# Kernel optimization log

Hardware: AMD Instinct MI355X
Metric: run time of the kernel (lower is better)

The kernel has to match this reference:

```python
import jax, jax.numpy as jnp
import numpy as np

NUM_TREE = 64
DEPTH = 7
INPUT_FEATURE = 1024
BATCH = 32768
LEAF = 2 ** (DEPTH - 1)  # 64


def setup_inputs() -> dict:
    key = jax.random.key(0)
    k1, k2 = jax.random.split(key, 2)
    x = jax.random.normal(k1, (BATCH, INPUT_FEATURE), dtype=jnp.float32)
    # each tree picks leaf_num-1 distinct feature columns (one-hot matmul == gather)
    rng = np.random.default_rng(0)
    idx = np.stack([rng.choice(INPUT_FEATURE, LEAF - 1, replace=False)
                    for _ in range(NUM_TREE)]).astype(np.int32)
    feature_idx = jnp.asarray(idx)  # [T, L-1]
    # pi.get_mean(): leaf means, np.random.rand -> uniform [0,1)
    pi = jax.random.uniform(k2, (NUM_TREE, LEAF), dtype=jnp.float32)
    return {"x": x, "feature_idx": feature_idx, "pi": pi}


def reference(x, feature_idx, pi):
    T, Lm1 = feature_idx.shape
    leaf = Lm1 + 1
    depth = int(np.log2(leaf)) + 1  # static
    B = x.shape[0]
    # torch.mm(x, one_hot_feature) == column gather; sigmoid routing decisions
    d = jax.nn.sigmoid(x[:, feature_idx])  # [B, T, L-1]
    # recursive cumulative-product leaf probabilities over tree layers (BFS order)
    mu = jnp.ones((B, T, 1), dtype=x.dtype)
    begin = 0
    for layer in range(depth - 1):
        n = 2 ** layer
        dl = d[:, :, begin:begin + n]  # [B, T, n]
        # child order per node: (left=sigmoid, right=1-sigmoid), interleaved
        mu = jnp.stack([mu * dl, mu * (1.0 - dl)], axis=-1).reshape(B, T, 2 * n)
        begin += n
    # mu: [B, T, L] leaf probabilities per tree
    prob = jnp.einsum('btl,tl->bt', mu, pi)        # [B, T]
    probs = jnp.transpose(mu, (0, 2, 1))           # [B, L, T] (matches torch layout)
    return prob, probs
```

## Files before the change

### kernel.cpp

```cpp
#include <hip/hip_runtime.h>

#define NTREE  64
#define NFEAT  1024
#define NLEAF  64
#define NBATCH 32768
#define WAVES  4
#define THREADS 256

__global__ __launch_bounds__(THREADS)
void forest_kernel(const float* __restrict__ x,
                   const int*   __restrict__ fidx,
                   const float* __restrict__ pi,
                   float* __restrict__ prob,
                   float* __restrict__ probs)
{
    __shared__ float srow[WAVES][NFEAT];
    __shared__ int   idxl[NTREE * 63];
    __shared__ float pil[NTREE * 65];

    const int tid  = threadIdx.x;
    const int wid  = tid >> 6;
    const int lane = tid & 63;

    for (int i = tid; i < NTREE * 63; i += THREADS) idxl[i] = fidx[i];
    for (int i = tid; i < NTREE * NLEAF; i += THREADS)
        pil[(i >> 6) * 65 + (i & 63)] = pi[i];
    __syncthreads();

    const int wavestride = gridDim.x * WAVES;
    for (int b = blockIdx.x * WAVES + wid; b < NBATCH; b += wavestride) {
        const float4* xr4 = reinterpret_cast<const float4*>(x + (size_t)b * NFEAT);
        float4* sr4 = reinterpret_cast<float4*>(&srow[wid][0]);
        #pragma unroll
        for (int i = 0; i < NFEAT / (64 * 4); ++i) {
            float4 v = xr4[lane + i * 64];
            float4 s;
            s.x = 1.0f / (1.0f + __expf(-v.x));
            s.y = 1.0f / (1.0f + __expf(-v.y));
            s.z = 1.0f / (1.0f + __expf(-v.z));
            s.w = 1.0f / (1.0f + __expf(-v.w));
            sr4[lane + i * 64] = s;
        }
        __syncthreads();

        const int t = lane;
        const float* sw = &srow[wid][0];
        const int ib = t * 63;

        float mu[32];
        mu[0] = 1.0f;
        #pragma unroll
        for (int k = 0; k < 5; ++k) {
            const int n = 1 << k;
            #pragma unroll
            for (int i = n - 1; i >= 0; --i) {
                float dv = sw[idxl[ib + (n - 1) + i]];
                float m  = mu[i];
                float a  = m * dv;
                mu[2 * i]     = a;
                mu[2 * i + 1] = m - a;
            }
        }

        float acc = 0.0f;
        float* pb = probs + (size_t)b * (NLEAF * NTREE) + t;
        const int ip = t * 65;
        #pragma unroll
        for (int i = 0; i < 32; ++i) {
            float dv = sw[idxl[ib + 31 + i]];
            float m  = mu[i];
            float a  = m * dv;
            float c  = m - a;
            pb[(2 * i) * NTREE]     = a;
            pb[(2 * i + 1) * NTREE] = c;
            acc = fmaf(a, pil[ip + 2 * i], acc);
            acc = fmaf(c, pil[ip + 2 * i + 1], acc);
        }
        prob[b * NTREE + t] = acc;
        __syncthreads();
    }
}

extern "C" void kernel_launch(void* const* d_in, const int* in_sizes, int n_in,
                              void* d_out, int out_size, void* d_ws, size_t ws_size,
                              hipStream_t stream) {
    const float* x    = (const float*)d_in[0];
    const int*   fidx = (const int*)d_in[1];
    const float* pi   = (const float*)d_in[2];
    float* prob  = (float*)d_out;
    float* probs = (float*)d_out + (size_t)NBATCH * NTREE;

    dim3 grid(2048), block(THREADS);
    hipLaunchKernelGGL(forest_kernel, grid, block, 0, stream,
                       x, fidx, pi, prob, probs);
}
```

Measured before the change: 137.7 us.

## Preload packed gather offsets into registers, drop per-row barriers, use fp16 pi

Packs the per-tree feature indices as pairs of 16-bit byte offsets that stay in registers, so the shared-memory index lookup before every gather goes away. It drops the per-row __syncthreads because each wave uses only its own row buffer. It rewrites the leaf dot product algebraically as m*(dv*(pi0-pi1)+pi1), with pi stored as half2 in a conflict-free layout. It also swaps the sigmoid division for a hardware reciprocal and adds an occupancy hint. The fp16 pi and approximate reciprocal reduce accuracy slightly, and the register-held offsets add register pressure.

```diff
diff --git a/kernel.cpp b/kernel.cpp
--- a/kernel.cpp
+++ b/kernel.cpp
@@ -1,4 +1,5 @@
 #include <hip/hip_runtime.h>
+#include <hip/hip_fp16.h>
 
 #define NTREE  64
 #define NFEAT  1024
@@ -6,46 +7,64 @@
 #define NBATCH 32768
 #define WAVES  4
 #define THREADS 256
+#define GRID   2048
+#define WSTRIDE (GRID * WAVES)
 
-__global__ __launch_bounds__(THREADS)
+__device__ __forceinline__ float sig1(float v) {
+    return __builtin_amdgcn_rcpf(1.0f + __expf(-v));
+}
+
+__global__ __launch_bounds__(THREADS, 5)
 void forest_kernel(const float* __restrict__ x,
                    const int*   __restrict__ fidx,
                    const float* __restrict__ pi,
                    float* __restrict__ prob,
                    float* __restrict__ probs)
 {
-    __shared__ float srow[WAVES][NFEAT];
-    __shared__ int   idxl[NTREE * 63];
-    __shared__ float pil[NTREE * 65];
+    __shared__ float   srow[WAVES][NFEAT];
+    __shared__ __half2 pil[32 * NTREE];
 
     const int tid  = threadIdx.x;
     const int wid  = tid >> 6;
     const int lane = tid & 63;
 
-    for (int i = tid; i < NTREE * 63; i += THREADS) idxl[i] = fidx[i];
-    for (int i = tid; i < NTREE * NLEAF; i += THREADS)
-        pil[(i >> 6) * 65 + (i & 63)] = pi[i];
+    unsigned* idxp = reinterpret_cast<unsigned*>(&srow[0][0]);
+    for (int i = tid; i < 2048; i += THREADS) {
+        int k = i >> 6, t = i & 63;
+        unsigned v0 = (unsigned)fidx[t * 63 + 2 * k] << 2;
+        unsigned v1 = (2 * k + 1 < 63) ? ((unsigned)fidx[t * 63 + 2 * k + 1] << 2) : 0u;
+        idxp[i] = v0 | (v1 << 16);
+    }
+    for (int i = tid; i < 2048; i += THREADS) {
+        int k = i >> 6, t = i & 63;
+        float p1 = pi[t * 64 + 2 * k + 1];
+        pil[i] = __floats2half2_rn(pi[t * 64 + 2 * k] - p1, p1);
+    }
     __syncthreads();
 
-    const int wavestride = gridDim.x * WAVES;
-    for (int b = blockIdx.x * WAVES + wid; b < NBATCH; b += wavestride) {
+    unsigned ioff[32];
+    const unsigned basep = (unsigned)(wid * (NFEAT * 4)) * 0x10001u;
+    #pragma unroll
+    for (int k = 0; k < 32; ++k) ioff[k] = idxp[k * 64 + lane] + basep;
+    __syncthreads();
+
+    const int t = lane;
+    char* swc = reinterpret_cast<char*>(&srow[0][0]);
+
+#define OFF(j)  ((j) & 1 ? (ioff[(j) >> 1] >> 16) : (ioff[(j) >> 1] & 0xFFFFu))
+#define GATH(j) (*reinterpret_cast<const float*>(swc + OFF(j)))
+
+    int b = blockIdx.x * WAVES + wid;
+    #pragma unroll 1
+    for (int it = 0; it < NBATCH / WSTRIDE; ++it, b += WSTRIDE) {
         const float4* xr4 = reinterpret_cast<const float4*>(x + (size_t)b * NFEAT);
         float4* sr4 = reinterpret_cast<float4*>(&srow[wid][0]);
         #pragma unroll
-        for (int i = 0; i < NFEAT / (64 * 4); ++i) {
+        for (int i = 0; i < 4; ++i) {
             float4 v = xr4[lane + i * 64];
-            float4 s;
-            s.x = 1.0f / (1.0f + __expf(-v.x));
-            s.y = 1.0f / (1.0f + __expf(-v.y));
-            s.z = 1.0f / (1.0f + __expf(-v.z));
-            s.w = 1.0f / (1.0f + __expf(-v.w));
-            sr4[lane + i * 64] = s;
+            sr4[lane + i * 64] =
+                make_float4(sig1(v.x), sig1(v.y), sig1(v.z), sig1(v.w));
         }
-        __syncthreads();
-
-        const int t = lane;
-        const float* sw = &srow[wid][0];
-        const int ib = t * 63;
 
         float mu[32];
         mu[0] = 1.0f;
@@ -54,7 +73,7 @@
             const int n = 1 << k;
             #pragma unroll
             for (int i = n - 1; i >= 0; --i) {
-                float dv = sw[idxl[ib + (n - 1) + i]];
+                float dv = GATH(n - 1 + i);
                 float m  = mu[i];
                 float a  = m * dv;
                 mu[2 * i]     = a;
@@ -64,21 +83,21 @@
 
         float acc = 0.0f;
         float* pb = probs + (size_t)b * (NLEAF * NTREE) + t;
-        const int ip = t * 65;
         #pragma unroll
         for (int i = 0; i < 32; ++i) {
-            float dv = sw[idxl[ib + 31 + i]];
+            float dv = GATH(31 + i);
             float m  = mu[i];
             float a  = m * dv;
             float c  = m - a;
             pb[(2 * i) * NTREE]     = a;
             pb[(2 * i + 1) * NTREE] = c;
-            acc = fmaf(a, pil[ip + 2 * i], acc);
-            acc = fmaf(c, pil[ip + 2 * i + 1], acc);
+            float2 p = __half22float2(pil[i * 64 + t]);
+            acc = fmaf(m, fmaf(dv, p.x, p.y), acc);
         }
         prob[b * NTREE + t] = acc;
-        __syncthreads();
     }
+#undef OFF
+#undef GATH
 }
 
 extern "C" void kernel_launch(void* const* d_in, const int* in_sizes, int n_in,
@@ -90,7 +109,7 @@
     float* prob  = (float*)d_out;
     float* probs = (float*)d_out + (size_t)NBATCH * NTREE;
 
-    dim3 grid(2048), block(THREADS);
+    dim3 grid(GRID), block(THREADS);
     hipLaunchKernelGGL(forest_kernel, grid, block, 0, stream,
                        x, fidx, pi, prob, probs);
 }
```

After: 174.6 us. +26.8%, slower.
